# Optimization experiments

Hardware: AMD Instinct MI355X
Metric: run time of the kernel (lower is better)

## Reference

```python
import jax, jax.numpy as jnp
import numpy as np

# --- static mask-construction config (mirrors FlexAttnFunc.init_mask args) ---
B = 1
L_F, L_H, L_W = 8, 20, 36      # latent_shape[2:]
A_F, A_H, A_W = 8, 1, 1        # action_shape[2:]
PATCH = (1, 2, 2)
CHUNK = 1
PAD = 176
WINDOW = 6
DIM, HEADS, DHEAD = 1536, 12, 128
EPS = 1e-5


def _make_ids():
    lf, lh, lw = L_F // PATCH[0], L_H // PATCH[1], L_W // PATCH[2]
    lat_seq = np.repeat(np.arange(B), lf * lh * lw)
    act_seq = np.repeat(np.arange(B), A_F * A_H * A_W)
    seq = np.concatenate([lat_seq, lat_seq, act_seq, act_seq])
    lat_fr = np.broadcast_to(np.arange(L_F)[None, :, None, None], (B, L_F, lh, lw)).reshape(-1)
    act_fr = np.broadcast_to(np.arange(A_F)[None, :, None, None], (B, A_F, A_H, A_W)).reshape(-1)
    fr = np.concatenate([lat_fr // CHUNK * 2] * 2 + [act_fr // CHUNK * 2 + 1] * 2)
    nz = np.concatenate([np.zeros_like(lat_fr), np.ones_like(lat_fr),
                         np.zeros_like(act_fr), np.ones_like(act_fr)])
    pad = np.full(PAD, -1, dtype=np.int64)
    return (np.concatenate([seq, pad]).astype(np.int32),
            np.concatenate([fr, pad]).astype(np.int32),
            np.concatenate([nz, pad]).astype(np.int32))


def setup_inputs() -> dict:
    key = jax.random.key(0)
    ks = jax.random.split(key, 8)
    seq, fr, nz = _make_ids()
    S = seq.shape[0]  # 3072
    sd = 0.02
    return {
        'x': jax.random.normal(ks[0], (1, S, DIM), jnp.float32),
        'Wq': jax.random.normal(ks[1], (DIM, DIM), jnp.float32) * sd,
        'bq': jnp.zeros((DIM,), jnp.float32),
        'Wk': jax.random.normal(ks[2], (DIM, DIM), jnp.float32) * sd,
        'bk': jnp.zeros((DIM,), jnp.float32),
        'Wv': jax.random.normal(ks[3], (DIM, DIM), jnp.float32) * sd,
        'bv': jnp.zeros((DIM,), jnp.float32),
        'gq': 1.0 + jax.random.normal(ks[4], (DIM,), jnp.float32) * sd,
        'gk': 1.0 + jax.random.normal(ks[5], (DIM,), jnp.float32) * sd,
        'Wo': jax.random.normal(ks[6], (DIM, DIM), jnp.float32) * sd,
        'bo': jnp.zeros((DIM,), jnp.float32),
        'seq_ids': jnp.asarray(seq),
        'frame_ids': jnp.asarray(fr),
        'noise_ids': jnp.asarray(nz),
        'window_size': WINDOW,
    }


def _rms(u, g):
    # torch.nn.RMSNorm over last dim (size heads*dim_head), elementwise affine
    return u * jax.lax.rsqrt(jnp.mean(u * u, axis=-1, keepdims=True) + EPS) * g


def _mask(seq_ids, frame_ids, noise_ids, window_size):
    sq, sk = seq_ids[:, None], seq_ids[None, :]
    fq, fk = frame_ids[:, None], frame_ids[None, :]
    nq, nk = noise_ids[:, None], noise_ids[None, :]
    seq_ok = (sq == sk) & (sq >= 0) & (sk >= 0)
    c2c = (nq == 1) & (nk == 1) & (fk <= fq)      # clean->clean, block causal incl self
    n2c = (nq == 0) & (nk == 1) & (fk < fq)       # noise->clean, causal excl self
    n2n = (nq == 0) & (nk == 0) & (fk == fq)      # noise->noise, same frame only
    win = jnp.abs(fq - fk) <= window_size
    return (c2c | n2c | n2n) & seq_ok & win


def reference(x, Wq, bq, Wk, bk, Wv, bv, gq, gk, Wo, bo,
              seq_ids, frame_ids, noise_ids, window_size):
    S = x.shape[1]
    q = _rms(x @ Wq + bq, gq)[0].reshape(S, HEADS, DHEAD)
    k = _rms(x @ Wk + bk, gk)[0].reshape(S, HEADS, DHEAD)
    v = (x @ Wv + bv)[0].reshape(S, HEADS, DHEAD)
    mask = _mask(seq_ids, frame_ids, noise_ids, window_size)  # [S,S] bool
    scores = jnp.einsum('qhd,khd->hqk', q, k) * (DHEAD ** -0.5)
    scores = jnp.where(mask[None], scores, jnp.float32(-1e9))
    attn = jax.nn.softmax(scores, axis=-1)
    o = jnp.einsum('hqk,khd->qhd', attn, v)
    # zero out padded (fully-masked) query rows
    o = o * (seq_ids >= 0).astype(o.dtype)[:, None, None]
    y = o.reshape(1, S, HEADS * DHEAD) @ Wo + bo
    return y
```

## Files before the change

kernel.cpp:

```cpp
#include <hip/hip_runtime.h>
#include <hip/hip_bf16.h>
#include <stdint.h>

typedef __bf16 bf16x8 __attribute__((ext_vector_type(8)));
typedef float f32x4 __attribute__((ext_vector_type(4)));

__device__ __forceinline__ unsigned short f2bf(float f) {
  union { float f; unsigned int u; } v; v.f = f;
  unsigned int u = v.u;
  unsigned int r = (u + 0x7fffu + ((u >> 16) & 1u)) >> 16;
  return (unsigned short)r;
}
__device__ __forceinline__ float bf2f(unsigned short s) {
  union { unsigned int u; float f; } v; v.u = ((unsigned int)s) << 16; return v.f;
}

__global__ __launch_bounds__(256) void setup(
    const float* __restrict__ x,
    const float* __restrict__ Wq, const float* __restrict__ Wk,
    const float* __restrict__ Wv, const float* __restrict__ Wo,
    const int* __restrict__ seq, const int* __restrict__ fr,
    const int* __restrict__ nz, const int* __restrict__ wsz,
    unsigned short* __restrict__ x_bf, unsigned short* __restrict__ wt,
    unsigned long long* __restrict__ tbm, unsigned char* __restrict__ mb,
    float* __restrict__ ssq, int S) {
  __shared__ __align__(16) unsigned char smu[16384];
  int b = blockIdx.x, tid = threadIdx.x;
  if (b < 1152) {
    int base = b * 1024 + tid;
    for (int j = 0; j < 4; j++) {
      int i = base + j * 256;
      float4 v = ((const float4*)x)[i];
      ushort4 o;
      o.x = f2bf(v.x); o.y = f2bf(v.y); o.z = f2bf(v.z); o.w = f2bf(v.w);
      ((ushort4*)x_bf)[i] = o;
    }
  } else if (b < 3456) {
    int id = b - 1152;
    int z = id / 576, rem = id % 576;
    int kx = rem % 24, ny = rem / 24;
    const float* W = z == 0 ? Wq : (z == 1 ? Wk : (z == 2 ? Wv : Wo));
    unsigned short (*t)[65] = (unsigned short(*)[65])smu;
    int k0 = kx * 64, n0 = ny * 64;
    const int N = 1536, K = 1536;
    for (int i = 0; i < 16; i++) {
      int e = tid + i * 256;
      int r = e >> 6, c = e & 63;
      t[r][c] = f2bf(W[(size_t)(k0 + r) * N + n0 + c]);
    }
    __syncthreads();
    for (int i = 0; i < 16; i++) {
      int e = tid + i * 256;
      int r = e >> 6, c = e & 63;
      wt[(size_t)(z * 1536 + n0 + r) * K + k0 + c] = t[c][r];
    }
  } else if (b == 3456) {
    int* ks_ = (int*)smu;
    unsigned int* tm_ = (unsigned int*)(smu + 12288);
    int W = wsz[0];
    for (int i = tid; i < S; i += 256) {
      int sq = seq[i];
      ks_[i] = (sq < 0) ? 0 : ((1 << 9) | ((nz[i] & 1) << 8) | (fr[i] & 15) | (sq << 10));
    }
    for (int i = tid; i < 6144; i += 256) ssq[i] = 0.f;
    __syncthreads();
    for (int t = tid; t < S / 32; t += 256) {
      unsigned int m = 0;
      for (int j = 0; j < 32; j++) {
        int a = ks_[t * 32 + j];
        if (a & (1 << 9)) m |= (a & (1 << 8)) ? (1u << (16 + (a & 15))) : (1u << (a & 15));
      }
      tm_[t] = m;
    }
    __syncthreads();
    for (int qg = tid; qg < S / 16; qg += 256) {
      unsigned int allowed = 0;
      for (int j = 0; j < 16; j++) {
        int a = ks_[qg * 16 + j];
        if (!(a & (1 << 9))) continue;
        int fq = a & 15, nq = (a >> 8) & 1;
        int lo = fq - W; if (lo < 0) lo = 0;
        unsigned int lom = ~((1u << lo) - 1);
        if (nq) allowed |= (((1u << (fq + 1)) - 1) & lom) << 16;
        else    allowed |= ((((1u << fq) - 1) & lom) << 16) | (1u << fq);
      }
      unsigned long long b0 = 0, b1 = 0;
      for (int t = 0; t < 96; t++)
        if (tm_[t] & allowed) { if (t < 64) b0 |= 1ull << t; else b1 |= 1ull << (t - 64); }
      tbm[qg * 2] = b0; tbm[qg * 2 + 1] = b1;
    }
  } else {
    int qg = b - 3457;
    int* ks_ = (int*)smu;
    int W = wsz[0];
    for (int i = tid; i < S; i += 256) {
      int sq = seq[i];
      ks_[i] = (sq < 0) ? 0 : ((1 << 9) | ((nz[i] & 1) << 8) | (fr[i] & 15) | (sq << 10));
    }
    __syncthreads();
    int wave = tid >> 6, lane = tid & 63, quad = lane >> 4, l16 = lane & 15;
    int aq[4];
    for (int r = 0; r < 4; r++) aq[r] = ks_[qg * 16 + quad * 4 + r];
    for (int t = wave; t < 96; t += 4) {
      int ak[2] = { ks_[t * 32 + l16], ks_[t * 32 + 16 + l16] };
      unsigned int byte = 0;
      for (int nt = 0; nt < 2; nt++) {
        int a = ak[nt];
        int kfr = a & 15, knz = (a >> 8) & 1, kvb = (a >> 9) & 1, ksq = a >> 10;
        for (int r = 0; r < 4; r++) {
          int bq_ = aq[r];
          int qfr = bq_ & 15, qnz = (bq_ >> 8) & 1, qvb = (bq_ >> 9) & 1, qsq = bq_ >> 10;
          bool ok  = qvb && kvb && (qsq == ksq);
          bool c2c = qnz && knz && (kfr <= qfr);
          bool n2c = !qnz && knz && (kfr < qfr);
          bool n2n = !qnz && !knz && (kfr == qfr);
          int df = qfr - kfr; df = df < 0 ? -df : df;
          if ((c2c || n2c || n2n) && ok && (df <= W)) byte |= 1u << (nt * 4 + r);
        }
      }
      mb[((size_t)qg * 96 + t) * 64 + lane] = (unsigned char)byte;
    }
  }
}

__global__ __launch_bounds__(512) void gemm_qkv(
    const unsigned short* __restrict__ A, const unsigned short* __restrict__ Bt,
    const float* __restrict__ bq, const float* __restrict__ bk, const float* __restrict__ bv,
    const float* __restrict__ gq, const float* __restrict__ gk,
    unsigned short* __restrict__ qt, unsigned short* __restrict__ ktb,
    unsigned short* __restrict__ vtb, float* __restrict__ ssq, int S) {
  __shared__ __align__(16) unsigned short smem[65536];
  int tid = threadIdx.x, wid = tid >> 6, lane = tid & 63;
  int quad = lane >> 4, l16 = lane & 15;
  int m0 = blockIdx.x * 256, n0 = blockIdx.y * 256;
  int wm = (wid >> 2) * 128;
  int wn = (wid & 3) * 64;
  int lr = lane >> 3;
  int lsw = ((lane & 7) ^ lr) * 8;
  int sx = l16 & 7;

  f32x4 acc[8][4] = {};

#define STAGEQ(t_, q_) do { \
    if ((t_) < 24) { \
      int b_ = (t_) & 1; \
      int k0_ = (t_) * 64; \
      unsigned short* ldsb = ((q_) < 2) ? (smem + b_ * 16384) : (smem + 32768 + b_ * 16384); \
      const unsigned short* gsrc = ((q_) < 2) ? A : Bt; \
      int rbase = ((q_) < 2) ? m0 : n0; \
      int lo8_ = ((q_) & 1) * 8; \
      for (int c_ = 0; c_ < 2; c_++) { \
        int chunk = lo8_ + c_ * 16 + wid; \
        const unsigned short* src = gsrc + (size_t)(rbase + chunk * 8 + lr) * 1536 + k0_ + lsw; \
        __builtin_amdgcn_global_load_lds( \
            (const __attribute__((address_space(1))) unsigned int*)src, \
            (__attribute__((address_space(3))) unsigned int*)(ldsb + chunk * 512 + lane * 8), 16, 0, 0); \
      } \
    } } while (0)

  STAGEQ(0, 0); STAGEQ(0, 1); STAGEQ(0, 2); STAGEQ(0, 3);
  STAGEQ(1, 0);
  asm volatile("s_waitcnt vmcnt(2)" ::: "memory");
  __builtin_amdgcn_s_barrier();
  __builtin_amdgcn_sched_barrier(0);

#define PHASE(p) do { \
    constexpr int q_ = (p) & 3; \
    constexpr int tb_ = (p) >> 2; \
    constexpr int k8_ = (q_ >> 1) * 4; \
    constexpr int mi0_ = (q_ & 1) * 4; \
    unsigned short* Ab = smem + tb_ * 16384; \
    unsigned short* Bb = smem + 32768 + tb_ * 16384; \
    int so_ = ((k8_ + quad) ^ sx) << 3; \
    if constexpr ((q_ & 1) == 0) { \
      for (int nj = 0; nj < 4; nj++) \
        bfr[nj] = *(const bf16x8*)&Bb[(wn + nj * 16 + l16) * 64 + so_]; \
    } \
    bf16x8 af[4]; \
    for (int ii = 0; ii < 4; ii++) \
      af[ii] = *(const bf16x8*)&Ab[(wm + (mi0_ + ii) * 16 + l16) * 64 + so_]; \
    STAGEQ(2 * i + kStT[p], kStQ[p]); \
    __builtin_amdgcn_sched_barrier(0); \
    __builtin_amdgcn_s_barrier(); \
    asm volatile("s_waitcnt lgkmcnt(0)" ::: "memory"); \
    __builtin_amdgcn_sched_barrier(0); \
    __builtin_amdgcn_s_setprio(1); \
    for (int ii = 0; ii < 4; ii++) \
      for (int nj = 0; nj < 4; nj++) \
        acc[mi0_ + ii][nj] = __builtin_amdgcn_mfma_f32_16x16x32_bf16(af[ii], bfr[nj], acc[mi0_ + ii][nj], 0, 0, 0); \
    __builtin_amdgcn_s_setprio(0); \
    if constexpr (q_ == 3) { asm volatile("s_waitcnt vmcnt(2)" ::: "memory"); } \
    __builtin_amdgcn_s_barrier(); \
    __builtin_amdgcn_sched_barrier(0); \
  } while (0)

  constexpr int kStT[8] = {1, 1, 1, 2, 2, 2, 2, 3};
  constexpr int kStQ[8] = {1, 2, 3, 0, 1, 2, 3, 0};

  for (int i = 0; i < 12; i++) {
    bf16x8 bfr[4];
    PHASE(0); PHASE(1); PHASE(2); PHASE(3);
    PHASE(4); PHASE(5); PHASE(6); PHASE(7);
  }
#undef PHASE
#undef STAGEQ

  int region = (n0 >= 3072) ? 2 : (n0 >= 1536 ? 1 : 0);
  int cbase = n0 - region * 1536;
  int hh0 = cbase >> 7;
  unsigned short* Cs = smem;
  if (region < 2) {
    const float* bias = region == 0 ? bq : bk;
    float* ssqp = ssq + region * 3072;
    float ss[8][4] = {};
    for (int nj = 0; nj < 4; nj++) {
      int col = wn + nj * 16 + l16;
      float b = bias[cbase + col];
      float G = (region == 1) ? gq[cbase + col] * gk[cbase + col] : 1.0f;
      for (int mi = 0; mi < 8; mi++)
        for (int r = 0; r < 4; r++) {
          float v = acc[mi][nj][r] + b;
          ss[mi][r] += v * v;
          Cs[(wm + mi * 16 + quad * 4 + r) * 256 + col] = f2bf(v * G);
        }
    }
    for (int mi = 0; mi < 8; mi++)
      for (int r = 0; r < 4; r++) {
        float v = ss[mi][r];
        for (int o = 1; o < 16; o <<= 1) v += __shfl_xor(v, o);
        if (l16 == 0)
          atomicAdd(&ssqp[m0 + wm + mi * 16 + quad * 4 + r], v);
      }
    __syncthreads();
    unsigned short* outb = (region == 0 ? qt : ktb);
    for (int p = 0; p < 16; p++) {
      int o = p * 4096 + tid * 8;
      int row = o >> 8, col = o & 255;
      size_t dst = (size_t)(hh0 + (col >> 7)) * 393216 + (size_t)(m0 + row) * 128 + (col & 127);
      *(uint4*)&outb[dst] = *(const uint4*)&Cs[o];
    }
  } else {
    for (int nj = 0; nj < 4; nj++) {
      int col = wn + nj * 16 + l16;
      float b = bv[cbase + col];
      int c8 = l16 * 8;
      for (int mi = 0; mi < 8; mi++)
        for (int r = 0; r < 4; r++) {
          int sp = wm + mi * 16 + quad * 4 + r;
          Cs[col * 256 + (sp ^ c8)] = f2bf(acc[mi][nj][r] + b);
        }
    }
    __syncthreads();
    for (int hh = 0; hh < 2; hh++) {
      unsigned short* outp = vtb + ((size_t)(hh0 + hh) * 96 + (m0 >> 5)) * 4096;
      for (int p = 0; p < 8; p++) {
        int o = p * 4096 + tid * 8;
        int tile = o >> 12, rem = o & 4095;
        int dd = rem >> 5, s31 = rem & 31;
        int laddr = (hh * 128 + dd) * 256 + ((tile * 32 + s31) ^ ((dd & 15) * 8));
        *(uint4*)&outp[o] = *(const uint4*)&Cs[laddr];
      }
    }
  }
}

__global__ __launch_bounds__(256) void gemm_wo(
    const unsigned short* __restrict__ A, const unsigned short* __restrict__ Bt,
    const float* __restrict__ bias, float* __restrict__ C, int M, int N, int K) {
  __shared__ __align__(16) unsigned short As[128 * 64];
  __shared__ __align__(16) unsigned short Bs[64 * 64];
  int tid = threadIdx.x, wave = tid >> 6, lane = tid & 63;
  int quad = lane >> 4, l16 = lane & 15;
  int m0 = blockIdx.x * 128, n0 = blockIdx.y * 64;
  int wm = (wave & 1) * 64, wn = (wave >> 1) * 32;
  int lr = lane >> 3;
  int lc = ((lane & 7) ^ lr) * 8;
  int sx = l16 & 7;
  f32x4 acc[4][2] = {};
  for (int k0 = 0; k0 < K; k0 += 64) {
    for (int c = 0; c < 4; c++) {
      int chunk = wave * 4 + c;
      int row = chunk * 8 + lr;
      const unsigned short* ga = &A[(size_t)(m0 + row) * K + k0 + lc];
      __builtin_amdgcn_global_load_lds(
          (const __attribute__((address_space(1))) unsigned int*)ga,
          (__attribute__((address_space(3))) unsigned int*)(As + chunk * 512), 16, 0, 0);
    }
    for (int c = 0; c < 2; c++) {
      int chunk = wave * 2 + c;
      int row = chunk * 8 + lr;
      const unsigned short* gb = &Bt[(size_t)(n0 + row) * K + k0 + lc];
      __builtin_amdgcn_global_load_lds(
          (const __attribute__((address_space(1))) unsigned int*)gb,
          (__attribute__((address_space(3))) unsigned int*)(Bs + chunk * 512), 16, 0, 0);
    }
    __syncthreads();
    for (int kk = 0; kk < 64; kk += 32) {
      int k8 = kk >> 3;
      int sw = ((k8 + quad) ^ sx) << 3;
      bf16x8 af[4], bfr[2];
      for (int i = 0; i < 4; i++)
        af[i] = *(const bf16x8*)&As[(wm + i * 16 + l16) * 64 + sw];
      for (int j = 0; j < 2; j++)
        bfr[j] = *(const bf16x8*)&Bs[(wn + j * 16 + l16) * 64 + sw];
      for (int i = 0; i < 4; i++)
        for (int j = 0; j < 2; j++)
          acc[i][j] = __builtin_amdgcn_mfma_f32_16x16x32_bf16(af[i], bfr[j], acc[i][j], 0, 0, 0);
    }
    __syncthreads();
  }
  for (int j = 0; j < 2; j++) {
    int col = n0 + wn + j * 16 + l16;
    float b = bias[col];
    for (int i = 0; i < 4; i++)
      for (int r = 0; r < 4; r++)
        C[(size_t)(m0 + wm + i * 16 + quad * 4 + r) * N + col] = acc[i][j][r] + b;
  }
}

__global__ __launch_bounds__(256) void attn(
    const unsigned short* __restrict__ qt,
    const unsigned short* __restrict__ kt,
    const unsigned short* __restrict__ vt,
    const unsigned char* __restrict__ mb,
    const unsigned long long* __restrict__ tbm,
    const float* __restrict__ ssq,
    unsigned short* __restrict__ op0b, unsigned short* __restrict__ op1b,
    float* __restrict__ lp, int S) {
  const int h = blockIdx.x;
  const int qb64 = blockIdx.y;
  const int split = blockIdx.z;
  int tid = threadIdx.x, wave = tid >> 6, lane = tid & 63;
  int quad = lane >> 4, l16 = lane & 15;
  const float scale = 0.088388347648318447f;

  __shared__ __align__(16) unsigned short Ks[2][4096];
  __shared__ __align__(16) unsigned short Vs[2][4096];
  __shared__ __align__(16) unsigned short pshare[4][16][40];

  int qg = qb64 * 4 + wave;
  unsigned long long bm0 = tbm[(qb64 * 4) * 2]     | tbm[(qb64 * 4 + 1) * 2] |
                           tbm[(qb64 * 4 + 2) * 2] | tbm[(qb64 * 4 + 3) * 2];
  unsigned long long bm1 = tbm[(qb64 * 4) * 2 + 1]     | tbm[(qb64 * 4 + 1) * 2 + 1] |
                           tbm[(qb64 * 4 + 2) * 2 + 1] | tbm[(qb64 * 4 + 3) * 2 + 1];
  unsigned long long wb0 = tbm[qg * 2], wb1 = tbm[qg * 2 + 1];

  const unsigned short* kth = kt + (size_t)h * 96 * 4096;
  const unsigned short* vth = vt + (size_t)h * 96 * 4096;
  const unsigned char* mbq = mb + (size_t)qg * 96 * 64;

  bf16x8 qf[4];
  {
    const unsigned short* qp = qt + ((size_t)(h * 192 + qg) * 16 + l16) * 128 + quad * 8;
    for (int ks = 0; ks < 4; ks++) qf[ks] = *(const bf16x8*)&qp[ks * 32];
  }
  float qs[4];
  for (int r = 0; r < 4; r++) {
    int row = qb64 * 64 + wave * 16 + quad * 4 + r;
    qs[r] = rsqrtf(ssq[row] * (1.0f / 1536.0f) + 1e-5f) * scale;
  }
  const float* ssk = ssq + 3072;

  f32x4 oacc[8] = {};
  f32x4 lacc = {};
  const __bf16 onebf = (__bf16)1.0f;
  const bf16x8 ones = {onebf, onebf, onebf, onebf, onebf, onebf, onebf, onebf};

#define POP(dst) do { \
    if (bm0) { dst = __builtin_ctzll(bm0); bm0 &= bm0 - 1; } \
    else if (bm1) { dst = 64 + __builtin_ctzll(bm1); bm1 &= bm1 - 1; } \
    else dst = -1; } while (0)

#define STAGE(t_, b_) do { \
    for (int j = 0; j < 2; j++) { \
      int slot = j * 256 + tid; \
      int key = slot >> 4, cc = slot & 15; \
      const unsigned short* src = kth + (size_t)(t_) * 4096 + key * 128 + (cc ^ (key & 15)) * 8; \
      __builtin_amdgcn_global_load_lds( \
          (const __attribute__((address_space(1))) unsigned int*)src, \
          (__attribute__((address_space(3))) unsigned int*)(&Ks[b_][0] + j * 2048 + wave * 512), \
          16, 0, 0); \
    } \
    for (int j = 0; j < 2; j++) { \
      int slot = j * 256 + tid; \
      int row = slot >> 2, cc = slot & 3; \
      const unsigned short* src = vth + (size_t)(t_) * 4096 + row * 32 + (cc ^ ((row >> 1) & 3)) * 8; \
      __builtin_amdgcn_global_load_lds( \
          (const __attribute__((address_space(1))) unsigned int*)src, \
          (__attribute__((address_space(3))) unsigned int*)(&Vs[b_][0] + j * 2048 + wave * 512), \
          16, 0, 0); \
    } } while (0)

  int t, dsc;
  if (split) POP(dsc);
  POP(t);
  unsigned int mbyte = 0;
  float kss0 = 0.f, kss1 = 0.f;
  if (t >= 0) {
    STAGE(t, 0);
    mbyte = mbq[t * 64 + lane];
    kss0 = ssk[t * 32 + l16]; kss1 = ssk[t * 32 + 16 + l16];
  }
  __syncthreads();
  int buf = 0;

  while (t >= 0) {
    POP(dsc);
    int tn; POP(tn);
    unsigned int mbyte2 = 0;
    float nss0 = 0.f, nss1 = 0.f;
    if (tn >= 0) {
      STAGE(tn, buf ^ 1);
      mbyte2 = mbq[tn * 64 + lane];
      nss0 = ssk[tn * 32 + l16]; nss1 = ssk[tn * 32 + 16 + l16];
    }

    bool live = (t < 64) ? ((wb0 >> t) & 1) : ((wb1 >> (t - 64)) & 1);
    if (live) {
      f32x4 sacc[2] = {};
      for (int nt = 0; nt < 2; nt++) {
        int key = nt * 16 + l16;
        for (int ks = 0; ks < 4; ks++) {
          int cc = (ks * 4 + quad) ^ l16;
          bf16x8 kf = *(const bf16x8*)&Ks[buf][(key * 16 + cc) * 8];
          sacc[nt] = __builtin_amdgcn_mfma_f32_16x16x32_bf16(qf[ks], kf, sacc[nt], 0, 0, 0);
        }
      }
      float ksc[2];
      ksc[0] = rsqrtf(kss0 * (1.0f / 1536.0f) + 1e-5f);
      ksc[1] = rsqrtf(kss1 * (1.0f / 1536.0f) + 1e-5f);
      for (int nt = 0; nt < 2; nt++)
        for (int r = 0; r < 4; r++) {
          float e = __expf(sacc[nt][r] * (qs[r] * ksc[nt]) - 16.0f);
          float p = ((mbyte >> (nt * 4 + r)) & 1) ? e : 0.0f;
          pshare[wave][quad * 4 + r][nt * 16 + l16] = f2bf(p);
        }
      __asm__ __volatile__("s_waitcnt lgkmcnt(0)" ::: "memory");
      bf16x8 pf = *(const bf16x8*)&pshare[wave][l16][quad * 8];
      for (int d = 0; d < 8; d++) {
        int row = d * 16 + l16;
        int cc = quad ^ ((l16 >> 1) & 3);
        bf16x8 vf = *(const bf16x8*)&Vs[buf][(row * 4 + cc) * 8];
        oacc[d] = __builtin_amdgcn_mfma_f32_16x16x32_bf16(pf, vf, oacc[d], 0, 0, 0);
      }
      lacc = __builtin_amdgcn_mfma_f32_16x16x32_bf16(pf, ones, lacc, 0, 0, 0);
    }
    __syncthreads();
    buf ^= 1;
    t = tn;
    mbyte = mbyte2;
    kss0 = nss0; kss1 = nss1;
  }
#undef POP
#undef STAGE

  unsigned short* po = split ? op1b : op0b;
  for (int r = 0; r < 4; r++) {
    int q = qb64 * 64 + wave * 16 + quad * 4 + r;
    float inv = (lacc[r] > 0.f) ? 1.0f / lacc[r] : 0.0f;
    for (int d = 0; d < 8; d++)
      po[((size_t)h * S + q) * 128 + d * 16 + l16] = f2bf(oacc[d][r] * inv);
    if (l16 == 0)
      lp[((size_t)split * 12 + h) * S + q] = lacc[r];
  }
}

__global__ __launch_bounds__(256) void combine(const unsigned short* __restrict__ op0b,
                                               const unsigned short* __restrict__ op1b,
                                               const float* __restrict__ lp,
                                               const int* __restrict__ seq,
                                               unsigned short* __restrict__ ob, int S) {
  int e4 = blockIdx.x * 256 + threadIdx.x;
  int idx = e4 * 4;
  int per_h = S * 128;
  int h = idx / per_h;
  int rem = idx - h * per_h;
  int q = rem >> 7, dd = rem & 127;
  float l0 = lp[(size_t)h * S + q], l1 = lp[(size_t)(12 + h) * S + q];
  float tot = l0 + l1;
  float ok = (seq[q] >= 0 && tot > 0.f) ? 1.0f / tot : 0.0f;
  float w0 = l0 * ok, w1 = l1 * ok;
  ushort4 a = ((const ushort4*)op0b)[e4];
  ushort4 b = ((const ushort4*)op1b)[e4];
  ushort4 o;
  o.x = f2bf(bf2f(a.x) * w0 + bf2f(b.x) * w1);
  o.y = f2bf(bf2f(a.y) * w0 + bf2f(b.y) * w1);
  o.z = f2bf(bf2f(a.z) * w0 + bf2f(b.z) * w1);
  o.w = f2bf(bf2f(a.w) * w0 + bf2f(b.w) * w1);
  *(ushort4*)&ob[(size_t)q * 1536 + h * 128 + dd] = o;
}

extern "C" void kernel_launch(void* const* d_in, const int* in_sizes, int n_in,
                              void* d_out, int out_size, void* d_ws, size_t ws_size,
                              hipStream_t stream) {
  const float* x  = (const float*)d_in[0];
  const float* Wq = (const float*)d_in[1];
  const float* bq = (const float*)d_in[2];
  const float* Wk = (const float*)d_in[3];
  const float* bk = (const float*)d_in[4];
  const float* Wv = (const float*)d_in[5];
  const float* bv = (const float*)d_in[6];
  const float* gq = (const float*)d_in[7];
  const float* gk = (const float*)d_in[8];
  const float* Wo = (const float*)d_in[9];
  const float* bo = (const float*)d_in[10];
  const int* seq  = (const int*)d_in[11];
  const int* fr   = (const int*)d_in[12];
  const int* nz   = (const int*)d_in[13];
  const int* wsz  = (const int*)d_in[14];
  float* out = (float*)d_out;
  const int S = in_sizes[11];
  const int D = 1536;

  char* ws = (char*)d_ws;
  size_t off = 0;
  unsigned short* x_bf = (unsigned short*)(ws + off); off += (size_t)S * D * 2;
  unsigned short* wt   = (unsigned short*)(ws + off); off += (size_t)4 * D * D * 2;
  unsigned short* qt   = (unsigned short*)(ws + off); off += (size_t)S * D * 2;
  unsigned short* ktb  = (unsigned short*)(ws + off); off += (size_t)S * D * 2;
  unsigned short* vtb  = (unsigned short*)(ws + off); off += (size_t)S * D * 2;
  unsigned short* o_bf = (unsigned short*)(ws + off); off += (size_t)S * D * 2;
  unsigned short* op0b = (unsigned short*)(ws + off); off += (size_t)S * D * 2;
  unsigned short* op1b = (unsigned short*)(ws + off); off += (size_t)S * D * 2;
  unsigned long long* tbm = (unsigned long long*)(ws + off); off += (size_t)(S / 16) * 16;
  unsigned char*  mbuf = (unsigned char*)(ws + off);  off += (size_t)(S / 16) * 96 * 64;
  float*          lp   = (float*)(ws + off);          off += (size_t)2 * 12 * S * 4;
  float*          ssq  = (float*)(ws + off);          off += (size_t)2 * 3072 * 4;

  dim3 blk(256);
  setup<<<dim3(3649), blk, 0, stream>>>(x, Wq, Wk, Wv, Wo, seq, fr, nz, wsz,
                                        x_bf, wt, tbm, mbuf, ssq, S);
  gemm_qkv<<<dim3(S / 256, 3 * D / 256), dim3(512), 0, stream>>>(x_bf, wt, bq, bk, bv, gq, gk,
                                                                 qt, ktb, vtb, ssq, S);
  attn<<<dim3(D / 128, S / 64, 2), blk, 0, stream>>>(qt, ktb, vtb, mbuf, tbm, ssq,
                                                     op0b, op1b, lp, S);
  combine<<<dim3(12 * S * 128 / 4 / 256), blk, 0, stream>>>(op0b, op1b, lp, seq, o_bf, S);
  gemm_wo<<<dim3(S / 128, D / 64), blk, 0, stream>>>(o_bf, wt + (size_t)3 * D * D,
                                                     bo, out, S, D, D);
}
```

Measured before the change: 272.5 us.

## Load K/V fragments directly from global per wave, dropping LDS staging

The attention kernel stops staging K and V tiles into double-buffered shared memory with block-wide barriers. Each wave now walks only its own live-tile bitmask and loads K and V fragments straight from global memory into registers. This removes the __syncthreads per tile and the wasted iterations on tiles that are dead for a given wave. In exchange, the four waves of a block no longer share loads, so global/L2 traffic can grow, and the double-buffer prefetch overlap is lost.

```diff
diff --git a/kernel.cpp b/kernel.cpp
--- a/kernel.cpp
+++ b/kernel.cpp
@@ -334,16 +334,10 @@
   int quad = lane >> 4, l16 = lane & 15;
   const float scale = 0.088388347648318447f;
 
-  __shared__ __align__(16) unsigned short Ks[2][4096];
-  __shared__ __align__(16) unsigned short Vs[2][4096];
   __shared__ __align__(16) unsigned short pshare[4][16][40];
 
   int qg = qb64 * 4 + wave;
-  unsigned long long bm0 = tbm[(qb64 * 4) * 2]     | tbm[(qb64 * 4 + 1) * 2] |
-                           tbm[(qb64 * 4 + 2) * 2] | tbm[(qb64 * 4 + 3) * 2];
-  unsigned long long bm1 = tbm[(qb64 * 4) * 2 + 1]     | tbm[(qb64 * 4 + 1) * 2 + 1] |
-                           tbm[(qb64 * 4 + 2) * 2 + 1] | tbm[(qb64 * 4 + 3) * 2 + 1];
-  unsigned long long wb0 = tbm[qg * 2], wb1 = tbm[qg * 2 + 1];
+  unsigned long long bm0 = tbm[qg * 2], bm1 = tbm[qg * 2 + 1];
 
   const unsigned short* kth = kt + (size_t)h * 96 * 4096;
   const unsigned short* vth = vt + (size_t)h * 96 * 4096;
@@ -371,88 +365,49 @@
     else if (bm1) { dst = 64 + __builtin_ctzll(bm1); bm1 &= bm1 - 1; } \
     else dst = -1; } while (0)
 
-#define STAGE(t_, b_) do { \
-    for (int j = 0; j < 2; j++) { \
-      int slot = j * 256 + tid; \
-      int key = slot >> 4, cc = slot & 15; \
-      const unsigned short* src = kth + (size_t)(t_) * 4096 + key * 128 + (cc ^ (key & 15)) * 8; \
-      __builtin_amdgcn_global_load_lds( \
-          (const __attribute__((address_space(1))) unsigned int*)src, \
-          (__attribute__((address_space(3))) unsigned int*)(&Ks[b_][0] + j * 2048 + wave * 512), \
-          16, 0, 0); \
-    } \
-    for (int j = 0; j < 2; j++) { \
-      int slot = j * 256 + tid; \
-      int row = slot >> 2, cc = slot & 3; \
-      const unsigned short* src = vth + (size_t)(t_) * 4096 + row * 32 + (cc ^ ((row >> 1) & 3)) * 8; \
-      __builtin_amdgcn_global_load_lds( \
-          (const __attribute__((address_space(1))) unsigned int*)src, \
-          (__attribute__((address_space(3))) unsigned int*)(&Vs[b_][0] + j * 2048 + wave * 512), \
-          16, 0, 0); \
-    } } while (0)
-
   int t, dsc;
   if (split) POP(dsc);
   POP(t);
-  unsigned int mbyte = 0;
-  float kss0 = 0.f, kss1 = 0.f;
-  if (t >= 0) {
-    STAGE(t, 0);
-    mbyte = mbq[t * 64 + lane];
-    kss0 = ssk[t * 32 + l16]; kss1 = ssk[t * 32 + 16 + l16];
-  }
-  __syncthreads();
-  int buf = 0;
 
   while (t >= 0) {
+    const unsigned short* kp = kth + (size_t)t * 4096 + (size_t)l16 * 128 + quad * 8;
+    bf16x8 kf[2][4];
+    for (int nt = 0; nt < 2; nt++)
+      for (int ks = 0; ks < 4; ks++)
+        kf[nt][ks] = *(const bf16x8*)&kp[nt * 2048 + ks * 32];
+    unsigned int mbyte = mbq[t * 64 + lane];
+    float kss0 = ssk[t * 32 + l16], kss1 = ssk[t * 32 + 16 + l16];
+
+    f32x4 sacc[2] = {};
+    for (int nt = 0; nt < 2; nt++)
+      for (int ks = 0; ks < 4; ks++)
+        sacc[nt] = __builtin_amdgcn_mfma_f32_16x16x32_bf16(qf[ks], kf[nt][ks], sacc[nt], 0, 0, 0);
+
+    const unsigned short* vp = vth + (size_t)t * 4096 + (size_t)l16 * 32 + quad * 8;
+    bf16x8 vf[8];
+    for (int d = 0; d < 8; d++)
+      vf[d] = *(const bf16x8*)&vp[d * 512];
+
+    float ksc0 = rsqrtf(kss0 * (1.0f / 1536.0f) + 1e-5f);
+    float ksc1 = rsqrtf(kss1 * (1.0f / 1536.0f) + 1e-5f);
+    for (int nt = 0; nt < 2; nt++) {
+      float kscv = nt == 0 ? ksc0 : ksc1;
+      for (int r = 0; r < 4; r++) {
+        float e = __expf(sacc[nt][r] * (qs[r] * kscv) - 16.0f);
+        float p = ((mbyte >> (nt * 4 + r)) & 1) ? e : 0.0f;
+        pshare[wave][quad * 4 + r][nt * 16 + l16] = f2bf(p);
+      }
+    }
+    __asm__ __volatile__("s_waitcnt lgkmcnt(0)" ::: "memory");
+    bf16x8 pf = *(const bf16x8*)&pshare[wave][l16][quad * 8];
+    for (int d = 0; d < 8; d++)
+      oacc[d] = __builtin_amdgcn_mfma_f32_16x16x32_bf16(pf, vf[d], oacc[d], 0, 0, 0);
+    lacc = __builtin_amdgcn_mfma_f32_16x16x32_bf16(pf, ones, lacc, 0, 0, 0);
+
     POP(dsc);
-    int tn; POP(tn);
-    unsigned int mbyte2 = 0;
-    float nss0 = 0.f, nss1 = 0.f;
-    if (tn >= 0) {
-      STAGE(tn, buf ^ 1);
-      mbyte2 = mbq[tn * 64 + lane];
-      nss0 = ssk[tn * 32 + l16]; nss1 = ssk[tn * 32 + 16 + l16];
-    }
-
-    bool live = (t < 64) ? ((wb0 >> t) & 1) : ((wb1 >> (t - 64)) & 1);
-    if (live) {
-      f32x4 sacc[2] = {};
-      for (int nt = 0; nt < 2; nt++) {
-        int key = nt * 16 + l16;
-        for (int ks = 0; ks < 4; ks++) {
-          int cc = (ks * 4 + quad) ^ l16;
-          bf16x8 kf = *(const bf16x8*)&Ks[buf][(key * 16 + cc) * 8];
-          sacc[nt] = __builtin_amdgcn_mfma_f32_16x16x32_bf16(qf[ks], kf, sacc[nt], 0, 0, 0);
-        }
-      }
-      float ksc[2];
-      ksc[0] = rsqrtf(kss0 * (1.0f / 1536.0f) + 1e-5f);
-      ksc[1] = rsqrtf(kss1 * (1.0f / 1536.0f) + 1e-5f);
-      for (int nt = 0; nt < 2; nt++)
-        for (int r = 0; r < 4; r++) {
-          float e = __expf(sacc[nt][r] * (qs[r] * ksc[nt]) - 16.0f);
-          float p = ((mbyte >> (nt * 4 + r)) & 1) ? e : 0.0f;
-          pshare[wave][quad * 4 + r][nt * 16 + l16] = f2bf(p);
-        }
-      __asm__ __volatile__("s_waitcnt lgkmcnt(0)" ::: "memory");
-      bf16x8 pf = *(const bf16x8*)&pshare[wave][l16][quad * 8];
-      for (int d = 0; d < 8; d++) {
-        int row = d * 16 + l16;
-        int cc = quad ^ ((l16 >> 1) & 3);
-        bf16x8 vf = *(const bf16x8*)&Vs[buf][(row * 4 + cc) * 8];
-        oacc[d] = __builtin_amdgcn_mfma_f32_16x16x32_bf16(pf, vf, oacc[d], 0, 0, 0);
-      }
-      lacc = __builtin_amdgcn_mfma_f32_16x16x32_bf16(pf, ones, lacc, 0, 0, 0);
-    }
-    __syncthreads();
-    buf ^= 1;
-    t = tn;
-    mbyte = mbyte2;
-    kss0 = nss0; kss1 = nss1;
+    POP(t);
   }
 #undef POP
-#undef STAGE
 
   unsigned short* po = split ? op1b : op0b;
   for (int r = 0; r < 4; r++) {
```

Result: slower. 318.8 us (+17.0%).
